# Performance work log

Hardware: AMD Instinct MI355X
Metric: run time of the kernel (lower is better)

## Reference

```python
import jax, jax.numpy as jnp
import numpy as np

B, L, HID = 1, 4096, 2048
H, P, N, CH, K = 64, 64, 128, 256, 4
INTER = H * P              # 4096 = num_heads * head_dim
CONV_DIM = INTER + 2 * N   # 4352
OUT_IN = 2 * (INTER + N) + H  # 8512, d_mlp == 0
DT_MIN, DT_MAX, EPS = 0.0, 100.0, 1e-5


def setup_inputs() -> dict:
    key = jax.random.key(0)
    ks = jax.random.split(key, 6)
    hidden_states = jax.random.normal(ks[0], (B, L, HID), jnp.float32)
    W_in = jax.random.normal(ks[1], (HID, OUT_IN), jnp.float32) * 0.02
    conv_w = jax.random.normal(ks[2], (K, CONV_DIM), jnp.float32) * 0.1
    conv_b = jnp.zeros((CONV_DIM,), jnp.float32)
    # dt_bias = softplus^{-1}(dt), dt ~ LogUniform[1e-3, 1e-1] (matches init_dt_bias)
    u = jax.random.uniform(ks[3], (H,))
    dt = jnp.exp(u * (jnp.log(0.1) - jnp.log(0.001)) + jnp.log(0.001))
    dt_bias = dt + jnp.log(-jnp.expm1(-dt))
    A_log = jnp.log(jax.random.uniform(ks[4], (H,), minval=1.0, maxval=16.0))
    D = jnp.ones((H,), jnp.float32)
    norm_weight = jnp.ones((INTER,), jnp.float32)
    W_out = jax.random.normal(ks[5], (INTER, HID), jnp.float32) * 0.02
    return dict(hidden_states=hidden_states, W_in=W_in, conv_w=conv_w, conv_b=conv_b,
                dt_bias=dt_bias, A_log=A_log, D=D, norm_weight=norm_weight, W_out=W_out)


def reference(hidden_states, W_in, conv_w, conv_b, dt_bias, A_log, D, norm_weight, W_out):
    Bsz, Ls, _ = hidden_states.shape
    nc = Ls // CH  # number of chunks

    zxbcdt = hidden_states @ W_in  # (b, l, 2*inter + 2*N + H); d_mlp = 0
    z, xBC, dt = jnp.split(zxbcdt, [INTER, 2 * INTER + 2 * N], axis=-1)

    # causal depthwise conv1d (left-pad K-1) + silu
    xp = jnp.pad(xBC, ((0, 0), (K - 1, 0), (0, 0)))
    xBC = sum(xp[:, k:k + Ls, :] * conv_w[k] for k in range(K)) + conv_b
    xBC = jax.nn.silu(xBC)
    x, Bt, Ct = jnp.split(xBC, [INTER, INTER + N], axis=-1)
    x = x.reshape(Bsz, Ls, H, P)

    dt = jnp.clip(jax.nn.softplus(dt + dt_bias), DT_MIN, DT_MAX)  # (b, l, h)
    A = -jnp.exp(A_log)  # (h,), negative

    # ---- chunked SSD (structured state-space duality) ----
    xc = x.reshape(Bsz, nc, CH, H, P)
    Bc = Bt.reshape(Bsz, nc, CH, N)   # shared across heads
    Cc = Ct.reshape(Bsz, nc, CH, N)
    dtc = dt.reshape(Bsz, nc, CH, H)
    xdt = xc * dtc[..., None]                     # discretized input
    dA = jnp.transpose(dtc * A, (0, 3, 1, 2))     # (b, h, c, l)
    A_cs = jnp.cumsum(dA, axis=-1)                # (b, h, c, l)

    # intra-chunk causal decay matrix L[i,j] = exp(sum_{j<k<=i} dA[k])
    seg = A_cs[..., :, None] - A_cs[..., None, :]
    tri = jnp.tril(jnp.ones((CH, CH), bool))
    Lmat = jnp.where(tri, jnp.exp(seg), 0.0)      # (b, h, c, l, s)
    Y_diag = jnp.einsum('bcln,bcsn,bhcls,bcshp->bclhp', Cc, Bc, Lmat, xdt)

    # per-chunk end states
    decay_states = jnp.exp(A_cs[..., -1:] - A_cs)  # (b, h, c, l)
    states = jnp.einsum('bcln,bhcl,bclhp->bchpn', Bc, decay_states, xdt)

    # inter-chunk recurrence via decay matrix over chunks (initial state = 0)
    chunk_end = A_cs[..., -1]                                     # (b, h, c)
    pad_cs = jnp.pad(jnp.cumsum(chunk_end, axis=-1), ((0, 0), (0, 0), (1, 0)))
    segc = pad_cs[..., :, None] - pad_cs[..., None, :]            # (b, h, c+1, c+1)
    tric = jnp.tril(jnp.ones((nc + 1, nc + 1), bool))
    decay_chunk = jnp.where(tric, jnp.exp(segc), 0.0)
    init = jnp.zeros((Bsz, 1, H, P, N), states.dtype)
    states = jnp.concatenate([init, states], axis=1)              # (b, c+1, h, p, n)
    new_states = jnp.einsum('bhzc,bchpn->bzhpn', decay_chunk, states)
    states_in = new_states[:, :-1]                                # state entering each chunk

    state_decay = jnp.exp(A_cs)  # (b, h, c, l)
    Y_off = jnp.einsum('bcln,bchpn,bhcl->bclhp', Cc, states_in, state_decay)

    y = (Y_diag + Y_off).reshape(Bsz, Ls, H, P)
    y = y + x * D[None, None, :, None]            # skip connection
    y = y.reshape(Bsz, Ls, INTER)

    # gated RMSNorm: rmsnorm(y * silu(z)) * weight  (fp32 internally)
    yf = y.astype(jnp.float32) * jax.nn.silu(z.astype(jnp.float32))
    var = jnp.mean(yf * yf, axis=-1, keepdims=True)
    yf = yf * jax.lax.rsqrt(var + EPS) * norm_weight
    y = yf.astype(hidden_states.dtype)

    return y @ W_out
```

## Files before the change

### kernel.cpp

```cpp
#include <hip/hip_runtime.h>
#include <hip/hip_bf16.h>
#include <math.h>

typedef __bf16 bf16x8 __attribute__((ext_vector_type(8)));
typedef float f32x4 __attribute__((ext_vector_type(4)));

#define GLOBAL_LOAD_LDS16(gptr, lptr) \
  __builtin_amdgcn_global_load_lds((const __attribute__((address_space(1))) void*)(gptr), \
                                   (__attribute__((address_space(3))) void*)(lptr), 16, 0, 0)

#define LGKM0 do { asm volatile("s_waitcnt lgkmcnt(0)" ::: "memory"); \
                   __builtin_amdgcn_sched_barrier(0); } while (0)
#define VMC4  asm volatile("s_waitcnt vmcnt(4)" ::: "memory")
#define VMC2  asm volatile("s_waitcnt vmcnt(2)" ::: "memory")
#define VMC0  asm volatile("s_waitcnt vmcnt(0)" ::: "memory")
#define BAR() __builtin_amdgcn_s_barrier()

__device__ __forceinline__ void tile_map(int bid, int nbx, int nby, int& bx, int& by) {
  int nwg = nbx * nby;
  int q = nwg >> 3, r = nwg & 7;
  int xcd = bid & 7, orig = bid >> 3;
  int wgid = (xcd < r ? xcd * (q + 1) : r * (q + 1) + (xcd - r) * q) + orig;
  int per = nbx << 3;
  int grp = wgid / per;
  int rem = wgid - grp * per;
  int g0 = grp << 3;
  int gm = nby - g0; if (gm > 8) gm = 8;
  by = g0 + rem % gm;
  bx = rem / gm;
}

template<int MODE>
__global__ __launch_bounds__(512, 2)
void gemm8_kernel(const __bf16* __restrict__ A, const __bf16* __restrict__ BT,
                  int M, int N, int K, int Ktot,
                  __bf16* __restrict__ out0, float* __restrict__ out2,
                  __bf16* yio, float* __restrict__ ssum,
                  const float* __restrict__ nwp)
{
  __shared__ __align__(16) __bf16 smA[2][2][8192];
  __shared__ __align__(16) __bf16 smB[2][2][8192];
  const int tid  = threadIdx.x;
  const int wave = tid >> 6, lane = tid & 63;
  const int quad = lane >> 4, l16 = lane & 15;
  const int wave_m = wave >> 2;
  const int wave_n = wave & 3;
  int bx, by;
  tile_map(blockIdx.y * gridDim.x + blockIdx.x, gridDim.x, gridDim.y, bx, by);
  const int mBase = by * 256;
  const int nBase = bx * 256;
  const int kb = (MODE == 3) ? blockIdx.z : 0;
  const int kStart = kb * K;

  auto stageA = [&](int buf, int half, int rd, int k0) {
    int p = (rd << 9) + tid;
    int row = p >> 3;
    int lc  = (p & 7) ^ (row & 7);
    const __bf16* gp = A + (size_t)(mBase + (half << 7) + row) * Ktot + k0 + (lc << 3);
    GLOBAL_LOAD_LDS16(gp, &smA[buf][half][(rd << 12) + (wave << 9)]);
  };
  auto stageB = [&](int buf, int half, int rd, int k0) {
    int p = (rd << 9) + tid;
    int row = p >> 3;
    int lc  = (p & 7) ^ (row & 7);
    const __bf16* gp = BT + (size_t)(nBase + (half << 7) + row) * Ktot + k0 + (lc << 3);
    GLOBAL_LOAD_LDS16(gp, &smB[buf][half][(rd << 12) + (wave << 9)]);
  };
  auto ldA = [&](int buf, int row, int chunk) -> bf16x8 {
    return *(const bf16x8*)(&smA[buf][wave_m][(row << 6) + (((chunk) ^ (row & 7)) << 3)]);
  };
  auto ldB = [&](int buf, int row, int chunk) -> bf16x8 {
    return *(const bf16x8*)(&smB[buf][wave_n >> 1][(row << 6) + (((chunk) ^ (row & 7)) << 3)]);
  };

  f32x4 acc[8][4] = {};
  const int nt = K / 64;

  {
    int k0 = kStart;
    stageB(0, 0, 0, k0); stageB(0, 0, 1, k0); stageB(0, 1, 0, k0); stageB(0, 1, 1, k0);
    stageA(0, 0, 0, k0); stageA(0, 1, 0, k0); stageA(0, 0, 1, k0); stageA(0, 1, 1, k0);
  }
  VMC2;
  BAR();

  const int browB = ((wave_n & 1) << 6);
  for (int U = 0; U < nt; ++U) {
    const int cur = U & 1, nb = cur ^ 1;
    const int k1 = kStart + (U + 1) * 64;
    const bool pf = (U + 1 < nt);
    bf16x8 af[4], b0[4], b1[4];

#pragma unroll
    for (int fi = 0; fi < 4; ++fi) af[fi] = ldA(cur, fi * 16 + l16, quad);
#pragma unroll
    for (int fj = 0; fj < 4; ++fj) b0[fj] = ldB(cur, browB + fj * 16 + l16, quad);
    if (pf) { stageB(nb, 0, 0, k1); stageB(nb, 0, 1, k1); }
    BAR();
    LGKM0;
    __builtin_amdgcn_s_setprio(1);
#pragma unroll
    for (int fi = 0; fi < 4; ++fi)
#pragma unroll
      for (int fj = 0; fj < 4; ++fj)
        acc[fi][fj] = __builtin_amdgcn_mfma_f32_16x16x32_bf16(af[fi], b0[fj], acc[fi][fj], 0, 0, 0);
    __builtin_amdgcn_s_setprio(0);
    BAR();

#pragma unroll
    for (int fi = 0; fi < 4; ++fi) af[fi] = ldA(cur, fi * 16 + l16, 4 + quad);
#pragma unroll
    for (int fj = 0; fj < 4; ++fj) b1[fj] = ldB(cur, browB + fj * 16 + l16, 4 + quad);
    if (pf) { stageB(nb, 1, 0, k1); stageB(nb, 1, 1, k1); VMC4; } else { VMC0; }
    BAR();
    LGKM0;
    __builtin_amdgcn_s_setprio(1);
#pragma unroll
    for (int fi = 0; fi < 4; ++fi)
#pragma unroll
      for (int fj = 0; fj < 4; ++fj)
        acc[fi][fj] = __builtin_amdgcn_mfma_f32_16x16x32_bf16(af[fi], b1[fj], acc[fi][fj], 0, 0, 0);
    __builtin_amdgcn_s_setprio(0);
    BAR();

#pragma unroll
    for (int fi = 0; fi < 4; ++fi) af[fi] = ldA(cur, 64 + fi * 16 + l16, quad);
    if (pf) { stageA(nb, 0, 0, k1); stageA(nb, 1, 0, k1); }
    BAR();
    LGKM0;
    __builtin_amdgcn_s_setprio(1);
#pragma unroll
    for (int fi = 0; fi < 4; ++fi)
#pragma unroll
      for (int fj = 0; fj < 4; ++fj)
        acc[4 + fi][fj] = __builtin_amdgcn_mfma_f32_16x16x32_bf16(af[fi], b0[fj], acc[4 + fi][fj], 0, 0, 0);
    __builtin_amdgcn_s_setprio(0);
    BAR();

#pragma unroll
    for (int fi = 0; fi < 4; ++fi) af[fi] = ldA(cur, 64 + fi * 16 + l16, 4 + quad);
    if (pf) { stageA(nb, 0, 1, k1); stageA(nb, 1, 1, k1); VMC2; }
    BAR();
    LGKM0;
    __builtin_amdgcn_s_setprio(1);
#pragma unroll
    for (int fi = 0; fi < 4; ++fi)
#pragma unroll
      for (int fj = 0; fj < 4; ++fj)
        acc[4 + fi][fj] = __builtin_amdgcn_mfma_f32_16x16x32_bf16(af[fi], b1[fj], acc[4 + fi][fj], 0, 0, 0);
    __builtin_amdgcn_s_setprio(0);
    BAR();
  }

  const int wmOff = wave_m * 128, wnOff = wave_n * 64;
  if (MODE == 2) {
#pragma unroll
    for (int fi = 0; fi < 8; ++fi)
#pragma unroll
      for (int r = 0; r < 4; ++r) {
        int row = mBase + wmOff + fi * 16 + quad * 4 + r;
        float sq = 0.f;
#pragma unroll
        for (int fj = 0; fj < 4; ++fj) {
          int col = nBase + wnOff + fj * 16 + l16;
          float v = acc[fi][fj][r];
          size_t idx = (size_t)row * 4096 + col;
          float y0 = (float)yio[idx];
          float zg = v / (1.f + expf(-v));
          float yf = y0 * zg;
          yio[idx] = (__bf16)(yf * nwp[col]);
          sq += yf * yf;
        }
        for (int m = 1; m < 16; m <<= 1) sq += __shfl_xor(sq, m, 64);
        if (l16 == 0) atomicAdd(&ssum[row], sq);
      }
  } else if (MODE == 3) {
#pragma unroll
    for (int fi = 0; fi < 8; ++fi)
#pragma unroll
      for (int r = 0; r < 4; ++r) {
        int row = mBase + wmOff + fi * 16 + quad * 4 + r;
        float s = rsqrtf(ssum[row] / 4096.f + 1e-5f);
#pragma unroll
        for (int fj = 0; fj < 4; ++fj) {
          int col = nBase + wnOff + fj * 16 + l16;
          float o = acc[fi][fj][r] * s;
          o = (o == o && fabsf(o) < 1e30f) ? o : 0.f;
          atomicAdd(&out2[(size_t)row * N + col], o);
        }
      }
  } else {
#pragma unroll
    for (int fi = 0; fi < 8; ++fi) {
      int rowl = wmOff + fi * 16 + quad * 4;
#pragma unroll
      for (int fj = 0; fj < 4; ++fj) {
        int col = nBase + wnOff + fj * 16 + l16;
#pragma unroll
        for (int r = 0; r < 4; ++r) {
          float v = acc[fi][fj][r];
          int row = mBase + rowl + r;
          if (col < 4352)       out0[(size_t)row * 4352 + col]        = (__bf16)v;
          else if (col < 4416)  out2[(size_t)row * 64 + (col - 4352)] = v;
        }
      }
    }
  }
}

__global__ __launch_bounds__(256)
void cast_kernel(const float* __restrict__ in, __bf16* __restrict__ out)
{
  size_t g = ((size_t)blockIdx.x * 256 + threadIdx.x) * 8;
  for (int j = 0; j < 8; ++j) out[g + j] = (__bf16)in[g + j];
}

__global__ __launch_bounds__(256)
void transpose_kernel(const float* __restrict__ in, __bf16* __restrict__ out,
                      int R, int C, int col0)
{
  __shared__ __bf16 tile[64][72];
  const int tid = threadIdx.x;
  const int r0 = blockIdx.y * 64, c0 = blockIdx.x * 64;
  const int tr = tid >> 3, tc = (tid & 7) * 8;
  for (int hh = 0; hh < 2; ++hh) {
    const float* gp = in + (size_t)(r0 + tr + hh * 32) * C + col0 + c0 + tc;
    for (int j = 0; j < 8; ++j) tile[tr + hh * 32][tc + j] = (__bf16)gp[j];
  }
  __syncthreads();
  for (int hh = 0; hh < 2; ++hh) {
    __bf16* op = out + (size_t)(c0 + tr + hh * 32) * R + r0 + tc;
    for (int j = 0; j < 8; ++j) op[j] = tile[tc + j][tr + hh * 32];
  }
}

__global__ __launch_bounds__(256)
void conv_silu_kernel(const __bf16* __restrict__ xBCraw, const float* __restrict__ conv_w,
                      const float* __restrict__ conv_b,
                      __bf16* __restrict__ xconv, __bf16* __restrict__ Bmat,
                      __bf16* __restrict__ Cmat, __bf16* __restrict__ BTr)
{
  int g = blockIdx.x * 256 + threadIdx.x;
  int t = g / 544;
  int c = (g % 544) * 8;
  float acc[8];
  for (int j = 0; j < 8; ++j) acc[j] = conv_b[c + j];
  for (int k = 0; k < 4; ++k) {
    int ts = t + k - 3;
    if (ts >= 0) {
      const __bf16* xp = xBCraw + (size_t)ts * 4352 + c;
      const float*  wp = conv_w + (size_t)k * 4352 + c;
      for (int j = 0; j < 8; ++j) acc[j] += (float)xp[j] * wp[j];
    }
  }
  for (int j = 0; j < 8; ++j) { float v = acc[j]; acc[j] = v / (1.f + expf(-v)); }
  if (c < 4096) {
    __bf16* op = xconv + (size_t)t * 4096 + c;
    for (int j = 0; j < 8; ++j) op[j] = (__bf16)acc[j];
  } else if (c < 4224) {
    int n = c - 4096;
    for (int j = 0; j < 8; ++j) {
      Bmat[(size_t)t * 128 + n + j] = (__bf16)acc[j];
      BTr[(size_t)(n + j) * 4096 + t] = (__bf16)acc[j];
    }
  } else {
    int n = c - 4224;
    for (int j = 0; j < 8; ++j) Cmat[(size_t)t * 128 + n + j] = (__bf16)acc[j];
  }
}

__global__ __launch_bounds__(256)
void dt_cumsum_kernel(const float* __restrict__ dtraw, const float* __restrict__ dt_bias,
                      const float* __restrict__ A_log, float* __restrict__ dtp,
                      float* __restrict__ csbuf)
{
  int h = blockIdx.x, cch = blockIdx.y, i = threadIdx.x;
  int t = cch * 256 + i;
  float x = dtraw[(size_t)t * 64 + h] + dt_bias[h];
  float sp = (x > 20.f) ? x : log1pf(expf(x));
  sp = fminf(fmaxf(sp, 0.f), 100.f);
  dtp[(size_t)t * 64 + h] = sp;
  float Ah = -expf(A_log[h]);
  __shared__ float s[256];
  s[i] = sp * Ah;
  __syncthreads();
  for (int off = 1; off < 256; off <<= 1) {
    float add = (i >= off) ? s[i - off] : 0.f;
    __syncthreads();
    s[i] += add;
    __syncthreads();
  }
  csbuf[(size_t)h * 4096 + t] = s[i];
}

__global__ __launch_bounds__(256)
void xdtT_kernel(const __bf16* __restrict__ xconv, const float* __restrict__ dtp,
                 __bf16* __restrict__ xdtT)
{
  __shared__ __bf16 tile[64][72];
  const int tid = threadIdx.x;
  const int t0 = blockIdx.y * 64, c0 = blockIdx.x * 64;
  const int tr = tid >> 3, tc = (tid & 7) * 8;
  const int h = (c0 + tc) >> 6;
  for (int hh = 0; hh < 2; ++hh) {
    int t = t0 + tr + hh * 32;
    float ds = dtp[(size_t)t * 64 + h];
    const __bf16* gp = xconv + (size_t)t * 4096 + c0 + tc;
    for (int j = 0; j < 8; ++j) tile[tr + hh * 32][tc + j] = (__bf16)((float)gp[j] * ds);
  }
  __syncthreads();
  for (int hh = 0; hh < 2; ++hh) {
    __bf16* op = xdtT + (size_t)(c0 + tr + hh * 32) * 4096 + t0 + tc;
    for (int j = 0; j < 8; ++j) op[j] = tile[tc + j][tr + hh * 32];
  }
}

__global__ __launch_bounds__(256)
void scores_kernel(const __bf16* __restrict__ Cmat, const __bf16* __restrict__ Bmat,
                   __bf16* __restrict__ scores)
{
  const int c = blockIdx.x;
  const int lb = blockIdx.y * 128, sb = blockIdx.z * 128;
  const int tid = threadIdx.x, wave = tid >> 6, lane = tid & 63;
  const int quad = lane >> 4, l16 = lane & 15;
  const int wl = (wave & 1) * 64, ws = (wave >> 1) * 64;
  f32x4 acc[4][4] = {};
  for (int k = 0; k < 4; ++k) {
    bf16x8 af[4], bfr[4];
    for (int i = 0; i < 4; ++i) {
      int tl = c * 256 + lb + wl + i * 16 + l16;
      af[i] = *(const bf16x8*)(Cmat + (size_t)tl * 128 + k * 32 + quad * 8);
    }
    for (int j = 0; j < 4; ++j) {
      int ts = c * 256 + sb + ws + j * 16 + l16;
      bfr[j] = *(const bf16x8*)(Bmat + (size_t)ts * 128 + k * 32 + quad * 8);
    }
    for (int i = 0; i < 4; ++i)
      for (int j = 0; j < 4; ++j)
        acc[i][j] = __builtin_amdgcn_mfma_f32_16x16x32_bf16(af[i], bfr[j], acc[i][j], 0, 0, 0);
  }
  for (int i = 0; i < 4; ++i)
    for (int j = 0; j < 4; ++j) {
      int lrow = lb + wl + i * 16 + quad * 4;
      int scol = sb + ws + j * 16 + l16;
      for (int r = 0; r < 4; ++r)
        scores[((size_t)c * 256 + lrow + r) * 256 + scol] = (__bf16)acc[i][j][r];
    }
}

__global__ __launch_bounds__(256)
void states_kernel(const __bf16* __restrict__ xdtT, const __bf16* __restrict__ BTr,
                   const float* __restrict__ csbuf, __bf16* __restrict__ chunk_states)
{
  const int c = blockIdx.x, h = blockIdx.y;
  const int tid = threadIdx.x, wave = tid >> 6, lane = tid & 63;
  const int quad = lane >> 4, l16 = lane & 15;
  __shared__ float decay[256];
  {
    float cs_end = csbuf[(size_t)h * 4096 + c * 256 + 255];
    decay[tid] = expf(fminf(cs_end - csbuf[(size_t)h * 4096 + c * 256 + tid], 0.f));
  }
  __syncthreads();
  const int wn = wave * 32;
  f32x4 acc[4][2] = {};
  for (int k = 0; k < 8; ++k) {
    bf16x8 af[4], bfr[2];
    for (int i = 0; i < 4; ++i) {
      int p = i * 16 + l16;
      af[i] = *(const bf16x8*)(xdtT + (size_t)(h * 64 + p) * 4096 + c * 256 + k * 32 + quad * 8);
    }
    for (int j = 0; j < 2; ++j) {
      int n = wn + j * 16 + l16;
      bf16x8 raw = *(const bf16x8*)(BTr + (size_t)n * 4096 + c * 256 + k * 32 + quad * 8);
      bf16x8 sc;
      for (int jj = 0; jj < 8; ++jj)
        sc[jj] = (__bf16)((float)raw[jj] * decay[k * 32 + quad * 8 + jj]);
      bfr[j] = sc;
    }
    for (int i = 0; i < 4; ++i)
      for (int j = 0; j < 2; ++j)
        acc[i][j] = __builtin_amdgcn_mfma_f32_16x16x32_bf16(af[i], bfr[j], acc[i][j], 0, 0, 0);
  }
  for (int i = 0; i < 4; ++i)
    for (int j = 0; j < 2; ++j) {
      int p = i * 16 + quad * 4;
      int n = wn + j * 16 + l16;
      for (int r = 0; r < 4; ++r)
        chunk_states[(((size_t)c * 64 + h) * 64 + p + r) * 128 + n] = (__bf16)acc[i][j][r];
    }
}

__global__ __launch_bounds__(256)
void scan_kernel(__bf16* states, const float* __restrict__ csbuf)
{
  size_t id = (size_t)blockIdx.x * 256 + threadIdx.x;
  int n = id & 127;
  int p = (int)((id >> 7) & 63);
  int h = (int)(id >> 13);
  float S = 0.f;
  for (int c = 0; c < 16; ++c) {
    size_t idx = (((size_t)c * 64 + h) * 64 + p) * 128 + n;
    float cst = (float)states[idx];
    states[idx] = (__bf16)S;
    float ce = csbuf[(size_t)h * 4096 + c * 256 + 255];
    S = S * expf(fminf(ce, 0.f)) + cst;
  }
}

__global__ __launch_bounds__(256)
void y_kernel(const __bf16* __restrict__ Cmat, const __bf16* __restrict__ states_in,
              const __bf16* __restrict__ scores, const __bf16* __restrict__ xdtT,
              const float* __restrict__ csbuf, const float* __restrict__ Dvec,
              __bf16* y)
{
  const int c = blockIdx.x, h = blockIdx.y;
  const int tid = threadIdx.x, wave = tid >> 6, lane = tid & 63;
  const int quad = lane >> 4, l16 = lane & 15;
  __shared__ float cs[256];
  cs[tid] = csbuf[(size_t)h * 4096 + c * 256 + tid];
  __syncthreads();
  const int wl = wave * 64;
  f32x4 acc[4][4] = {};

  for (int k = 0; k < 4; ++k) {
    bf16x8 af[4], bfr[4];
    for (int i = 0; i < 4; ++i) {
      int tl = c * 256 + wl + i * 16 + l16;
      af[i] = *(const bf16x8*)(Cmat + (size_t)tl * 128 + k * 32 + quad * 8);
    }
    for (int j = 0; j < 4; ++j) {
      int p = j * 16 + l16;
      bfr[j] = *(const bf16x8*)(states_in + (((size_t)c * 64 + h) * 64 + p) * 128 + k * 32 + quad * 8);
    }
    for (int i = 0; i < 4; ++i)
      for (int j = 0; j < 4; ++j)
        acc[i][j] = __builtin_amdgcn_mfma_f32_16x16x32_bf16(af[i], bfr[j], acc[i][j], 0, 0, 0);
  }
  for (int i = 0; i < 4; ++i)
    for (int r = 0; r < 4; ++r) {
      float sd = expf(fminf(cs[wl + i * 16 + quad * 4 + r], 0.f));
      for (int j = 0; j < 4; ++j) acc[i][j][r] *= sd;
    }
  for (int sb = 0; sb < 8; ++sb) {
    bf16x8 af[4], bfr[4];
    for (int i = 0; i < 4; ++i) {
      int lloc = wl + i * 16 + l16;
      bf16x8 raw = *(const bf16x8*)(scores + ((size_t)c * 256 + lloc) * 256 + sb * 32 + quad * 8);
      float csl = cs[lloc];
      bf16x8 w;
      for (int jj = 0; jj < 8; ++jj) {
        int s = sb * 32 + quad * 8 + jj;
        float e = expf(fminf(csl - cs[s], 0.f));
        float v = (s <= lloc) ? (float)raw[jj] * e : 0.f;
        w[jj] = (__bf16)v;
      }
      af[i] = w;
    }
    for (int j = 0; j < 4; ++j) {
      int p = j * 16 + l16;
      bfr[j] = *(const bf16x8*)(xdtT + (size_t)(h * 64 + p) * 4096 + c * 256 + sb * 32 + quad * 8);
    }
    for (int i = 0; i < 4; ++i)
      for (int j = 0; j < 4; ++j)
        acc[i][j] = __builtin_amdgcn_mfma_f32_16x16x32_bf16(af[i], bfr[j], acc[i][j], 0, 0, 0);
  }
  float Dh = Dvec[h];
  for (int i = 0; i < 4; ++i)
    for (int r = 0; r < 4; ++r) {
      int tl = c * 256 + wl + i * 16 + quad * 4 + r;
      for (int j = 0; j < 4; ++j) {
        int p = j * 16 + l16;
        size_t idx = (size_t)tl * 4096 + h * 64 + p;
        float xv = (float)y[idx];
        y[idx] = (__bf16)(acc[i][j][r] + xv * Dh);
      }
    }
}

extern "C" void kernel_launch(void* const* d_in, const int* in_sizes, int n_in,
                              void* d_out, int out_size, void* d_ws, size_t ws_size,
                              hipStream_t stream)
{
  const float* hs      = (const float*)d_in[0];
  const float* W_in    = (const float*)d_in[1];
  const float* conv_w  = (const float*)d_in[2];
  const float* conv_b  = (const float*)d_in[3];
  const float* dt_bias = (const float*)d_in[4];
  const float* A_log   = (const float*)d_in[5];
  const float* Dv      = (const float*)d_in[6];
  const float* nw      = (const float*)d_in[7];
  const float* W_out   = (const float*)d_in[8];
  float* out = (float*)d_out;

  char* base = (char*)d_ws;
  const size_t P0 = 0;
  const size_t P1 = 35651584;
  const size_t P2 = 69206016;
  const size_t P3 = 77611008;

  __bf16* xBCraw  = (__bf16*)(base + P0);
  __bf16* xdtT    = (__bf16*)(base + P0);
  __bf16* wTz     = (__bf16*)(base + P0);
  __bf16* wT_out  = (__bf16*)(base + P0);
  __bf16* wTa     = (__bf16*)(base + P1);
  __bf16* xconv   = (__bf16*)(base + P1);
  __bf16* Bmat    = (__bf16*)(base + P2);
  __bf16* Cmat    = (__bf16*)(base + P2 + 1048576);
  __bf16* BTr     = (__bf16*)(base + P2 + 2097152);
  float*  dtp     = (float*) (base + P2 + 3145728);
  float*  csbuf   = (float*) (base + P2 + 4194304);
  __bf16* scores  = (__bf16*)(base + P2 + 5242880);
  float*  dtraw   = (float*) (base + P2 + 7340032);
  float*  ssum    = (float*) (base + P2 + 8388608);
  __bf16* hs16    = (__bf16*)(base + P3);
  __bf16* states  = (__bf16*)d_out;

  hipMemsetAsync(ssum, 0, 4096 * sizeof(float), stream);
  cast_kernel<<<4096, 256, 0, stream>>>(hs, hs16);
  transpose_kernel<<<dim3(69, 32), 256, 0, stream>>>(W_in, wTa, 2048, 8512, 4096);
  hipMemsetAsync(wTa + (size_t)4416 * 2048, 0, (size_t)192 * 2048 * 2, stream);
  gemm8_kernel<0><<<dim3(18, 16), 512, 0, stream>>>(hs16, wTa, 4096, 4416, 2048, 2048,
                                                    xBCraw, dtraw, nullptr, nullptr, nullptr);
  conv_silu_kernel<<<8704, 256, 0, stream>>>(xBCraw, conv_w, conv_b, xconv, Bmat, Cmat, BTr);
  dt_cumsum_kernel<<<dim3(64, 16), 256, 0, stream>>>(dtraw, dt_bias, A_log, dtp, csbuf);
  xdtT_kernel<<<dim3(64, 64), 256, 0, stream>>>(xconv, dtp, xdtT);
  scores_kernel<<<dim3(16, 2, 2), 256, 0, stream>>>(Cmat, Bmat, scores);
  states_kernel<<<dim3(16, 64), 256, 0, stream>>>(xdtT, BTr, csbuf, states);
  scan_kernel<<<2048, 256, 0, stream>>>(states, csbuf);
  y_kernel<<<dim3(16, 64), 256, 0, stream>>>(Cmat, states, scores, xdtT, csbuf, Dv, xconv);
  hipMemsetAsync(out, 0, (size_t)4096 * 2048 * 4, stream);
  transpose_kernel<<<dim3(64, 32), 256, 0, stream>>>(W_in, wTz, 2048, 8512, 0);
  gemm8_kernel<2><<<dim3(16, 16), 512, 0, stream>>>(hs16, wTz, 4096, 4096, 2048, 2048,
                                                    nullptr, nullptr, xconv, ssum, nw);
  transpose_kernel<<<dim3(32, 64), 256, 0, stream>>>(W_out, wT_out, 4096, 2048, 0);
  gemm8_kernel<3><<<dim3(8, 16, 2), 512, 0, stream>>>(xconv, wT_out, 4096, 2048, 2048, 4096,
                                                      nullptr, out, nullptr, ssum, nullptr);
}
```

Baseline: 670.2 us.

## Split in-projection GEMM tail into a separate kernel and drop manual LDS waits

The first projection GEMM now covers only the 4096 columns that tile evenly. A new, smaller 128x128-tile kernel computes the remaining xBC/dt columns, using a swizzled LDS layout and direct global-to-LDS loads. This is meant to cut the wasted padded work and the uneven extra tiles of the large tiled GEMM, at the cost of one more launch and an unpipelined tail kernel. The explicit lgkmcnt(0) waits and their sched barriers are also removed from the main GEMM loop. That leaves LDS wait placement to the compiler so it can overlap reads with MFMA issue.

```diff
diff --git a/kernel.cpp b/kernel.cpp
--- a/kernel.cpp
+++ b/kernel.cpp
@@ -9,8 +9,6 @@
   __builtin_amdgcn_global_load_lds((const __attribute__((address_space(1))) void*)(gptr), \
                                    (__attribute__((address_space(3))) void*)(lptr), 16, 0, 0)
 
-#define LGKM0 do { asm volatile("s_waitcnt lgkmcnt(0)" ::: "memory"); \
-                   __builtin_amdgcn_sched_barrier(0); } while (0)
 #define VMC4  asm volatile("s_waitcnt vmcnt(4)" ::: "memory")
 #define VMC2  asm volatile("s_waitcnt vmcnt(2)" ::: "memory")
 #define VMC0  asm volatile("s_waitcnt vmcnt(0)" ::: "memory")
@@ -28,6 +26,10 @@
   int gm = nby - g0; if (gm > 8) gm = 8;
   by = g0 + rem % gm;
   bx = rem / gm;
+}
+
+__device__ __forceinline__ int swz_off(int r, int quad) {
+  return ((r >> 1) << 6) + (((((r & 1) << 2) | quad) ^ ((r >> 1) & 7)) << 3);
 }
 
 template<int MODE>
@@ -97,7 +99,6 @@
     for (int fj = 0; fj < 4; ++fj) b0[fj] = ldB(cur, browB + fj * 16 + l16, quad);
     if (pf) { stageB(nb, 0, 0, k1); stageB(nb, 0, 1, k1); }
     BAR();
-    LGKM0;
     __builtin_amdgcn_s_setprio(1);
 #pragma unroll
     for (int fi = 0; fi < 4; ++fi)
@@ -113,7 +114,6 @@
     for (int fj = 0; fj < 4; ++fj) b1[fj] = ldB(cur, browB + fj * 16 + l16, 4 + quad);
     if (pf) { stageB(nb, 1, 0, k1); stageB(nb, 1, 1, k1); VMC4; } else { VMC0; }
     BAR();
-    LGKM0;
     __builtin_amdgcn_s_setprio(1);
 #pragma unroll
     for (int fi = 0; fi < 4; ++fi)
@@ -127,7 +127,6 @@
     for (int fi = 0; fi < 4; ++fi) af[fi] = ldA(cur, 64 + fi * 16 + l16, quad);
     if (pf) { stageA(nb, 0, 0, k1); stageA(nb, 1, 0, k1); }
     BAR();
-    LGKM0;
     __builtin_amdgcn_s_setprio(1);
 #pragma unroll
     for (int fi = 0; fi < 4; ++fi)
@@ -141,7 +140,6 @@
     for (int fi = 0; fi < 4; ++fi) af[fi] = ldA(cur, 64 + fi * 16 + l16, 4 + quad);
     if (pf) { stageA(nb, 0, 1, k1); stageA(nb, 1, 1, k1); VMC2; }
     BAR();
-    LGKM0;
     __builtin_amdgcn_s_setprio(1);
 #pragma unroll
     for (int fi = 0; fi < 4; ++fi)
@@ -200,9 +198,60 @@
         for (int r = 0; r < 4; ++r) {
           float v = acc[fi][fj][r];
           int row = mBase + rowl + r;
-          if (col < 4352)       out0[(size_t)row * 4352 + col]        = (__bf16)v;
-          else if (col < 4416)  out2[(size_t)row * 64 + (col - 4352)] = v;
+          out0[(size_t)row * 4352 + col] = (__bf16)v;
         }
+      }
+    }
+  }
+}
+
+__global__ __launch_bounds__(256, 3)
+void gemm_rem_kernel(const __bf16* __restrict__ A, const __bf16* __restrict__ BT,
+                     int Ktot, int colOff,
+                     __bf16* __restrict__ out0, float* __restrict__ out2)
+{
+  __shared__ __align__(16) __bf16 As[128 * 32];
+  __shared__ __align__(16) __bf16 Bs[128 * 32];
+  const int tid  = threadIdx.x;
+  const int wave = tid >> 6, lane = tid & 63;
+  const int quad = lane >> 4, l16 = lane & 15;
+  const int mBase = blockIdx.y * 128;
+  const int nBase = blockIdx.x * 128;
+  const int wm = (wave & 1) * 64;
+  const int wn = (wave >> 1) * 64;
+  f32x4 acc[4][4] = {};
+  for (int k0 = 0; k0 < Ktot; k0 += 32) {
+    __syncthreads();
+    for (int rd = 0; rd < 2; ++rd) {
+      int p = tid + rd * 256;
+      int rp = p >> 3, wi = p & 7;
+      int sp = wi ^ (rp & 7);
+      int srow = rp * 2 + (sp >> 2);
+      int sc8 = (sp & 3) * 8;
+      const __bf16* gpA = A + (size_t)(mBase + srow) * Ktot + k0 + sc8;
+      GLOBAL_LOAD_LDS16(gpA, As + rd * 2048 + wave * 512);
+      const __bf16* gpB = BT + (size_t)(nBase + srow) * Ktot + k0 + sc8;
+      GLOBAL_LOAD_LDS16(gpB, Bs + rd * 2048 + wave * 512);
+    }
+    __syncthreads();
+    bf16x8 af[4], bfr[4];
+    for (int i = 0; i < 4; ++i)
+      af[i] = *(const bf16x8*)(As + swz_off(wm + i * 16 + l16, quad));
+    for (int j = 0; j < 4; ++j)
+      bfr[j] = *(const bf16x8*)(Bs + swz_off(wn + j * 16 + l16, quad));
+    for (int i = 0; i < 4; ++i)
+      for (int j = 0; j < 4; ++j)
+        acc[i][j] = __builtin_amdgcn_mfma_f32_16x16x32_bf16(af[i], bfr[j], acc[i][j], 0, 0, 0);
+  }
+  for (int i = 0; i < 4; ++i) {
+    int rowl = wm + i * 16 + quad * 4;
+    for (int j = 0; j < 4; ++j) {
+      int col = colOff + nBase + wn + j * 16 + l16;
+      for (int r = 0; r < 4; ++r) {
+        float v = acc[i][j][r];
+        int row = mBase + rowl + r;
+        if (col < 4352)       out0[(size_t)row * 4352 + col]        = (__bf16)v;
+        else if (col < 4416)  out2[(size_t)row * 64 + (col - 4352)] = v;
       }
     }
   }
@@ -519,8 +568,10 @@
   cast_kernel<<<4096, 256, 0, stream>>>(hs, hs16);
   transpose_kernel<<<dim3(69, 32), 256, 0, stream>>>(W_in, wTa, 2048, 8512, 4096);
   hipMemsetAsync(wTa + (size_t)4416 * 2048, 0, (size_t)192 * 2048 * 2, stream);
-  gemm8_kernel<0><<<dim3(18, 16), 512, 0, stream>>>(hs16, wTa, 4096, 4416, 2048, 2048,
+  gemm8_kernel<0><<<dim3(16, 16), 512, 0, stream>>>(hs16, wTa, 4096, 4096, 2048, 2048,
                                                     xBCraw, dtraw, nullptr, nullptr, nullptr);
+  gemm_rem_kernel<<<dim3(3, 32), 256, 0, stream>>>(hs16, wTa + (size_t)4096 * 2048, 2048, 4096,
+                                                   xBCraw, dtraw);
   conv_silu_kernel<<<8704, 256, 0, stream>>>(xBCraw, conv_w, conv_b, xconv, Bmat, Cmat, BTr);
   dt_cumsum_kernel<<<dim3(64, 16), 256, 0, stream>>>(dtraw, dt_bias, A_log, dtp, csbuf);
   xdtT_kernel<<<dim3(64, 64), 256, 0, stream>>>(xconv, dtp, xdtT);
```

New measurement: 730.9 us. +9.1%, slower.
